# Performance work log

Hardware: AMD Instinct MI355X
Metric: run time of the kernel (lower is better)

Reference implementation:

```python
import jax, jax.numpy as jnp
import numpy as np
import math

B = 32
TS_LEN = 8192
DSEG = 32
S = TS_LEN // DSEG          # 256 segments
DM = 256                    # dim_model
NBITS = 8                   # bits of the bucket signature (synthetic _compute_index)
NBUCKETS = 2 ** NBITS       # 256 ragged-vocab buckets, made uniform here
W = 512                     # words per bucket (uniform -> vocabulary_dist[b] = b*W)
NHAAR = 6                   # min(log2(S)=8, max_haar_depth=6)
LMAX = 13                   # full haar depth of wavedec on length-8192 signal


def _layer_norm(x, eps=1e-5):
    m = x.mean(-1, keepdims=True)
    v = ((x - m) ** 2).mean(-1, keepdims=True)
    return (x - m) / jnp.sqrt(v + eps)


def _pos_emb():
    # sinusoidal positional embedding, matches the torch buffer construction
    pos = jnp.arange(S, dtype=jnp.float32)[:, None]
    div = jnp.exp(jnp.arange(0, DM, 2, dtype=jnp.float32) * (-math.log(10000.0) / DM))
    pe = jnp.zeros((S, DM), jnp.float32)
    pe = pe.at[:, 0::2].set(jnp.sin(pos * div))
    pe = pe.at[:, 1::2].set(jnp.cos(pos * div))
    return pe


def setup_inputs() -> dict:
    key = jax.random.key(0)
    k1, k2, k3, k4 = jax.random.split(key, 4)
    x = jax.random.normal(k1, (B, TS_LEN), jnp.float32)
    # candidate words live in [0,1] (they are compared against min-max-normalized segments)
    vocab_table = jax.random.uniform(k2, (NBUCKETS, W, DSEG), dtype=jnp.float32)
    word_emb = jax.random.normal(k3, (NBUCKETS * W, DM), jnp.float32)
    haar_emb = jax.random.normal(k4, (NHAAR + 1, DM), jnp.float32)
    return {"x": x, "vocab_table": vocab_table, "word_emb": word_emb, "haar_emb": haar_emb}


def reference(x, vocab_table, word_emb, haar_emb):
    # ---- _adjust: input length == ts_len -> identity, att_mask all ones ----
    att_mask = jnp.ones((B, S), jnp.int32)

    # ---- compute_word_embedding (vectorized over batch and segments) ----
    segs = x.reshape(B, S, DSEG)
    smin = segs.min(-1, keepdims=True)
    smax = segs.max(-1, keepdims=True)
    seg_norm = (segs - smin) / (smax - smin + 1e-8)
    # synthetic _compute_index: 8-bit signature (chunk mean above segment mean)
    chunk_means = segs.reshape(B, S, NBITS, DSEG // NBITS).mean(-1)       # [B,S,8]
    bits = (chunk_means > segs.mean(-1, keepdims=True)).astype(jnp.int32)
    bucket = (bits * (2 ** jnp.arange(NBITS, dtype=jnp.int32))).sum(-1)   # [B,S]
    cand = vocab_table[bucket]                                            # [B,S,W,DSEG]
    dist = jnp.abs(cand - seg_norm[:, :, None, :]).sum(-1)                # [B,S,W] L1 cdist
    best = jnp.argmin(dist, axis=-1)                                      # [B,S]
    word_embed = word_emb[bucket * W + best]                              # [B,S,DM]

    # ---- compute_haar_embedding (pywt.wavedec with 'haar', first NHAAR+1 coeffs) ----
    a = x
    details = []
    sqrt2 = jnp.float32(math.sqrt(2.0))
    for _ in range(LMAX):
        even = a[:, 0::2]
        odd = a[:, 1::2]
        details.append((even - odd) / sqrt2)
        a = (even + odd) / sqrt2
    coeffs = [a] + details[::-1]                # [cA_L, cD_L, ..., cD_1]
    taken = coeffs[: NHAAR + 1]
    rows = [jnp.repeat(c, S // c.shape[1], axis=1) for c in taken]        # each [B,S]
    haar_matrix = jnp.stack(rows, axis=-1)                                # [B,S,NHAAR+1]
    haar_matrix = haar_matrix * att_mask[..., None].astype(haar_matrix.dtype)
    haar_embed = haar_matrix @ haar_emb                                   # [B,S,DM]
    haar_embed = _layer_norm(haar_embed)

    out = word_embed + haar_embed + _pos_emb()
    out = _layer_norm(out)
    return (out, att_mask)
```

## Files before the change

### kernel.cpp

```cpp
#include <hip/hip_runtime.h>
#include <math.h>

#define BB 32
#define TS 8192
#define DSEG 32
#define SS 256
#define DM 256
#define W 512
#define CAP 1024

__global__ __launch_bounds__(256) void prep_haar_pe_kernel(
    const float* __restrict__ x,
    float* __restrict__ segn_g,
    unsigned char* __restrict__ bucketc,
    unsigned long long* __restrict__ bestkey,
    float* __restrict__ hout,
    float* __restrict__ pe_g)
{
    const int blk = blockIdx.x;
    const int t = threadIdx.x;

    if (blk < 1024) {
        const int segBase = blk * 8;
        __shared__ float sseg[8][32];
        sseg[t >> 5][t & 31] = x[(size_t)segBase * 32 + t];
        __syncthreads();

        const int hw = t >> 5;
        const int h = hw & 1;
        const int l = t & 31;
        const int seg = segBase + hw;

        float v = sseg[hw][l];
        float mn = v, mx = v, sm = v;
#pragma unroll
        for (int m = 1; m <= 16; m <<= 1) {
            mn = fminf(mn, __shfl_xor(mn, m));
            mx = fmaxf(mx, __shfl_xor(mx, m));
            sm += __shfl_xor(sm, m);
        }
        float mean = sm * (1.0f / 32.0f);
        float cm = 0.0f;
        if (l < 8) {
            cm = ((sseg[hw][4 * l] + sseg[hw][4 * l + 1]) + sseg[hw][4 * l + 2]) +
                 sseg[hw][4 * l + 3];
            cm *= 0.25f;
        }
        unsigned long long bal = __ballot(l < 8 && cm > mean);
        segn_g[(size_t)seg * 32 + l] = (v - mn) / (mx - mn + 1e-8f);
        if (l == 0) bucketc[seg] = (unsigned char)((bal >> (h * 32)) & 0xFF);
        if (l == 1) bestkey[seg] = ~0ULL;
    } else if (blk < 1056) {
        const int b = blk - 1024;
        const int lane = t;
        if (lane >= 64) return;
        const float* xb = x + (size_t)b * TS + (size_t)lane * 128;
        const float is2 = 0.70710678118654752440f;

        float a[64];
#pragma unroll
        for (int i = 0; i < 32; ++i) {
            float4 u = *(const float4*)(xb + 4 * i);
            a[2 * i + 0] = (u.x + u.y) * is2;
            a[2 * i + 1] = (u.z + u.w) * is2;
        }
#pragma unroll
        for (int len = 64; len > 1; len >>= 1) {
#pragma unroll
            for (int j = 0; j < (len >> 1); ++j)
                a[j] = (a[2 * j] + a[2 * j + 1]) * is2;
        }
        float val = a[0];
        float* ob = hout + b * 64;
#pragma unroll
        for (int len = 64; len > 1; len >>= 1) {
            float e = __shfl(val, 2 * lane);
            float o = __shfl(val, 2 * lane + 1);
            int half = len >> 1;
            if (lane < half) {
                ob[half + lane] = (e - o) * is2;
                val = (e + o) * is2;
            }
        }
        if (lane == 0) ob[0] = val;
    } else {
        const int s = blk - 1056;
        const float cexp = -9.210340371976184f / 256.0f;
        float dv = expf((float)(t & ~1) * cexp);
        float ang = (float)s * dv;
        pe_g[s * DM + t] = (t & 1) ? cosf(ang) : sinf(ang);
    }
}

__global__ __launch_bounds__(512) void search_kernel(
    const float* __restrict__ vocab,
    const float* __restrict__ segn_g,
    const unsigned char* __restrict__ bucketc,
    unsigned long long* __restrict__ bestkey)
{
    const int bucket = blockIdx.x >> 1;
    const int half = blockIdx.x & 1;
    const int t = threadIdx.x;
    const int lane = t & 63;
    const int wid = t >> 6;

    __shared__ float vsh[256 * 32];
    __shared__ int list[CAP];
    __shared__ int cnt;
    if (t == 0) cnt = 0;
    __syncthreads();

    {
        uint4 v16 = ((const uint4*)bucketc)[t];
        const unsigned char* pb = (const unsigned char*)&v16;
        int base = t * 16;
#pragma unroll
        for (int j = 0; j < 16; ++j) {
            if (pb[j] == (unsigned char)bucket) {
                int p = atomicAdd(&cnt, 1);
                if (p < CAP) list[p] = base + j;
            }
        }
    }

    const float* vb = vocab + ((size_t)bucket * W + (size_t)half * 256) * DSEG;
#pragma unroll 2
    for (int f = t; f < 2048; f += 512) {
        int r = f >> 3, q = f & 7;
        float4 u = ((const float4*)vb)[f];
        int sq = q ^ (r & 7);
        *(float4*)&vsh[r * 32 + sq * 4] = u;
    }
    __syncthreads();

    int n = cnt; if (n > CAP) n = CAP;
    for (int i = 2 * wid; i < n; i += 16) {
        const int segA = list[i];
        const bool hasB = (i + 1 < n);
        const int segB = hasB ? list[i + 1] : segA;
        const float* spA = segn_g + (size_t)segA * 32;
        const float* spB = segn_g + (size_t)segB * 32;
        float svA[32], svB[32];
#pragma unroll
        for (int d = 0; d < 32; ++d) { svA[d] = spA[d]; svB[d] = spB[d]; }

        unsigned long long bestA = ~0ULL, bestB = ~0ULL;
#pragma unroll
        for (int c = 0; c < 4; ++c) {
            const int r = c * 64 + lane;
            float dA = 0.0f, dB = 0.0f;
#pragma unroll
            for (int q = 0; q < 8; ++q) {
                float4 u = *(const float4*)&vsh[r * 32 + ((q ^ (r & 7)) * 4)];
                dA += fabsf(u.x - svA[4 * q + 0]);
                dA += fabsf(u.y - svA[4 * q + 1]);
                dA += fabsf(u.z - svA[4 * q + 2]);
                dA += fabsf(u.w - svA[4 * q + 3]);
                dB += fabsf(u.x - svB[4 * q + 0]);
                dB += fabsf(u.y - svB[4 * q + 1]);
                dB += fabsf(u.z - svB[4 * q + 2]);
                dB += fabsf(u.w - svB[4 * q + 3]);
            }
            unsigned w = (unsigned)(half * 256 + r);
            unsigned long long kA =
                ((unsigned long long)__float_as_uint(dA) << 32) | w;
            unsigned long long kB =
                ((unsigned long long)__float_as_uint(dB) << 32) | w;
            if (kA < bestA) bestA = kA;
            if (kB < bestB) bestB = kB;
        }
#pragma unroll
        for (int m = 1; m < 64; m <<= 1) {
            unsigned long long oA = __shfl_xor(bestA, m);
            unsigned long long oB = __shfl_xor(bestB, m);
            if (oA < bestA) bestA = oA;
            if (oB < bestB) bestB = oB;
        }
        if (lane == 0) {
            atomicMin(bestkey + segA, bestA);
            if (hasB) atomicMin(bestkey + segB, bestB);
        }
    }
}

__global__ __launch_bounds__(256) void out_kernel(
    const float* __restrict__ wemb,
    const float* __restrict__ hemb,
    const float* __restrict__ hcoef,
    const float* __restrict__ pe_g,
    const unsigned char* __restrict__ bucketc,
    const unsigned long long* __restrict__ bestkey,
    float* __restrict__ out)
{
    const int bs = (blockIdx.x << 2) + (threadIdx.x >> 6);
    const int lane = threadIdx.x & 63;
    const int b = bs >> 8;
    const int s = bs & 255;

    const int bucket = bucketc[bs];
    const int bestw = (int)(unsigned)(bestkey[bs] & 0xFFFFFFFFull);

    const float* hb = hcoef + b * 64;
    float hk[7];
    hk[0] = hb[0];
#pragma unroll
    for (int k = 1; k <= 6; ++k)
        hk[k] = hb[(1 << (k - 1)) + (s >> (8 - (k - 1)))];

    float h0 = 0.f, h1 = 0.f, h2 = 0.f, h3 = 0.f;
#pragma unroll
    for (int k = 0; k < 7; ++k) {
        float4 he = ((const float4*)(hemb + k * DM))[lane];
        h0 += hk[k] * he.x; h1 += hk[k] * he.y;
        h2 += hk[k] * he.z; h3 += hk[k] * he.w;
    }

    float sm = ((h0 + h1) + h2) + h3;
    float sq = ((h0 * h0 + h1 * h1) + h2 * h2) + h3 * h3;
#pragma unroll
    for (int m = 1; m < 64; m <<= 1) {
        sm += __shfl_xor(sm, m);
        sq += __shfl_xor(sq, m);
    }
    float mh = sm * (1.0f / 256.0f);
    float vh = fmaxf(sq * (1.0f / 256.0f) - mh * mh, 0.0f);
    float rs = 1.0f / sqrtf(vh + 1e-5f);
    float n0 = (h0 - mh) * rs, n1 = (h1 - mh) * rs;
    float n2 = (h2 - mh) * rs, n3 = (h3 - mh) * rs;

    const size_t row = (size_t)bucket * W + (size_t)bestw;
    float4 wv = ((const float4*)(wemb + row * DM))[lane];

    float4 pv = ((const float4*)(pe_g + s * DM))[lane];

    float o0 = wv.x + n0 + pv.x;
    float o1 = wv.y + n1 + pv.y;
    float o2 = wv.z + n2 + pv.z;
    float o3 = wv.w + n3 + pv.w;

    float sm2 = ((o0 + o1) + o2) + o3;
    float sq2 = ((o0 * o0 + o1 * o1) + o2 * o2) + o3 * o3;
#pragma unroll
    for (int m = 1; m < 64; m <<= 1) {
        sm2 += __shfl_xor(sm2, m);
        sq2 += __shfl_xor(sq2, m);
    }
    float mo = sm2 * (1.0f / 256.0f);
    float vo = fmaxf(sq2 * (1.0f / 256.0f) - mo * mo, 0.0f);
    float rs2 = 1.0f / sqrtf(vo + 1e-5f);

    float4 res;
    res.x = (o0 - mo) * rs2; res.y = (o1 - mo) * rs2;
    res.z = (o2 - mo) * rs2; res.w = (o3 - mo) * rs2;
    ((float4*)(out + (size_t)bs * DM))[lane] = res;
    if (lane == 0) out[(size_t)BB * SS * DM + bs] = 1.0f;
}

extern "C" void kernel_launch(void* const* d_in, const int* in_sizes, int n_in,
                              void* d_out, int out_size, void* d_ws, size_t ws_size,
                              hipStream_t stream) {
    const float* x     = (const float*)d_in[0];
    const float* vocab = (const float*)d_in[1];
    const float* wemb  = (const float*)d_in[2];
    const float* hemb  = (const float*)d_in[3];
    float* out = (float*)d_out;

    char* ws = (char*)d_ws;
    float* segn                  = (float*)ws;
    unsigned long long* bestkey  = (unsigned long long*)(ws + 1048576);
    unsigned char* bucketc       = (unsigned char*)(ws + 1048576 + 65536);
    float* hco                   = (float*)(ws + 1048576 + 65536 + 8192);
    float* pe_g                  = (float*)(ws + 1048576 + 65536 + 16384);

    prep_haar_pe_kernel<<<1312, 256, 0, stream>>>(x, segn, bucketc, bestkey,
                                                  hco, pe_g);
    search_kernel<<<512, 512, 0, stream>>>(vocab, segn, bucketc, bestkey);
    out_kernel<<<2048, 256, 0, stream>>>(wemb, hemb, hco, pe_g, bucketc,
                                         bestkey, out);
}
```

Before: 206.9 us.

## Build per-bucket segment lists in prep kernel and split search eightfold

The prep kernel now appends each segment to a global per-bucket list through an atomic counter, zeroed by a memset, so the search kernel no longer scans all bucket bytes in every block. The search is split into 8 blocks per bucket, each holding 64 candidate words in shared memory, which gives 2048 smaller blocks with more parallelism and less shared memory per block. The cost is an extra memset launch, more global atomics on bucket counters, and each segment's data being reloaded by 8 blocks instead of 2.

Result: slower. 232.8 us (+12.6%).

```diff
diff --git a/kernel.cpp b/kernel.cpp
--- a/kernel.cpp
+++ b/kernel.cpp
@@ -7,7 +7,9 @@
 #define SS 256
 #define DM 256
 #define W 512
-#define CAP 1024
+#define SPLIT 8
+#define CAND (W / SPLIT)
+#define CAP 2048
 
 __global__ __launch_bounds__(256) void prep_haar_pe_kernel(
     const float* __restrict__ x,
@@ -15,7 +17,9 @@
     unsigned char* __restrict__ bucketc,
     unsigned long long* __restrict__ bestkey,
     float* __restrict__ hout,
-    float* __restrict__ pe_g)
+    float* __restrict__ pe_g,
+    int* __restrict__ bucket_cnt,
+    int* __restrict__ list_g)
 {
     const int blk = blockIdx.x;
     const int t = threadIdx.x;
@@ -48,7 +52,12 @@
         }
         unsigned long long bal = __ballot(l < 8 && cm > mean);
         segn_g[(size_t)seg * 32 + l] = (v - mn) / (mx - mn + 1e-8f);
-        if (l == 0) bucketc[seg] = (unsigned char)((bal >> (h * 32)) & 0xFF);
+        if (l == 0) {
+            int bucket = (int)((bal >> (h * 32)) & 0xFF);
+            bucketc[seg] = (unsigned char)bucket;
+            int slot = atomicAdd(bucket_cnt + bucket, 1);
+            if (slot < CAP) list_g[bucket * CAP + slot] = seg;
+        }
         if (l == 1) bestkey[seg] = ~0ULL;
     } else if (blk < 1056) {
         const int b = blk - 1024;
@@ -95,80 +104,62 @@
 __global__ __launch_bounds__(512) void search_kernel(
     const float* __restrict__ vocab,
     const float* __restrict__ segn_g,
-    const unsigned char* __restrict__ bucketc,
+    const int* __restrict__ bucket_cnt,
+    const int* __restrict__ list_g,
     unsigned long long* __restrict__ bestkey)
 {
-    const int bucket = blockIdx.x >> 1;
-    const int half = blockIdx.x & 1;
+    const int bucket = blockIdx.x >> 3;
+    const int part = blockIdx.x & 7;
     const int t = threadIdx.x;
     const int lane = t & 63;
     const int wid = t >> 6;
 
-    __shared__ float vsh[256 * 32];
-    __shared__ int list[CAP];
-    __shared__ int cnt;
-    if (t == 0) cnt = 0;
-    __syncthreads();
+    __shared__ float vsh[CAND * 32];
 
     {
-        uint4 v16 = ((const uint4*)bucketc)[t];
-        const unsigned char* pb = (const unsigned char*)&v16;
-        int base = t * 16;
-#pragma unroll
-        for (int j = 0; j < 16; ++j) {
-            if (pb[j] == (unsigned char)bucket) {
-                int p = atomicAdd(&cnt, 1);
-                if (p < CAP) list[p] = base + j;
-            }
-        }
-    }
-
-    const float* vb = vocab + ((size_t)bucket * W + (size_t)half * 256) * DSEG;
-#pragma unroll 2
-    for (int f = t; f < 2048; f += 512) {
-        int r = f >> 3, q = f & 7;
-        float4 u = ((const float4*)vb)[f];
+        const float* vb =
+            vocab + ((size_t)bucket * W + (size_t)part * CAND) * DSEG;
+        int r = t >> 3, q = t & 7;
+        float4 u = ((const float4*)vb)[t];
         int sq = q ^ (r & 7);
         *(float4*)&vsh[r * 32 + sq * 4] = u;
     }
+    int n = bucket_cnt[bucket];
+    if (n > CAP) n = CAP;
     __syncthreads();
-
-    int n = cnt; if (n > CAP) n = CAP;
+    if (n == 0) return;
+
+    const int* lst = list_g + bucket * CAP;
+    const unsigned wbase = (unsigned)(part * CAND);
+
     for (int i = 2 * wid; i < n; i += 16) {
-        const int segA = list[i];
+        const int segA = lst[i];
         const bool hasB = (i + 1 < n);
-        const int segB = hasB ? list[i + 1] : segA;
+        const int segB = hasB ? lst[i + 1] : segA;
         const float* spA = segn_g + (size_t)segA * 32;
         const float* spB = segn_g + (size_t)segB * 32;
         float svA[32], svB[32];
 #pragma unroll
         for (int d = 0; d < 32; ++d) { svA[d] = spA[d]; svB[d] = spB[d]; }
 
-        unsigned long long bestA = ~0ULL, bestB = ~0ULL;
-#pragma unroll
-        for (int c = 0; c < 4; ++c) {
-            const int r = c * 64 + lane;
-            float dA = 0.0f, dB = 0.0f;
-#pragma unroll
-            for (int q = 0; q < 8; ++q) {
-                float4 u = *(const float4*)&vsh[r * 32 + ((q ^ (r & 7)) * 4)];
-                dA += fabsf(u.x - svA[4 * q + 0]);
-                dA += fabsf(u.y - svA[4 * q + 1]);
-                dA += fabsf(u.z - svA[4 * q + 2]);
-                dA += fabsf(u.w - svA[4 * q + 3]);
-                dB += fabsf(u.x - svB[4 * q + 0]);
-                dB += fabsf(u.y - svB[4 * q + 1]);
-                dB += fabsf(u.z - svB[4 * q + 2]);
-                dB += fabsf(u.w - svB[4 * q + 3]);
-            }
-            unsigned w = (unsigned)(half * 256 + r);
-            unsigned long long kA =
-                ((unsigned long long)__float_as_uint(dA) << 32) | w;
-            unsigned long long kB =
-                ((unsigned long long)__float_as_uint(dB) << 32) | w;
-            if (kA < bestA) bestA = kA;
-            if (kB < bestB) bestB = kB;
-        }
+        const int r = lane;
+        float dA = 0.0f, dB = 0.0f;
+#pragma unroll
+        for (int q = 0; q < 8; ++q) {
+            float4 u = *(const float4*)&vsh[r * 32 + ((q ^ (r & 7)) * 4)];
+            dA += fabsf(u.x - svA[4 * q + 0]);
+            dA += fabsf(u.y - svA[4 * q + 1]);
+            dA += fabsf(u.z - svA[4 * q + 2]);
+            dA += fabsf(u.w - svA[4 * q + 3]);
+            dB += fabsf(u.x - svB[4 * q + 0]);
+            dB += fabsf(u.y - svB[4 * q + 1]);
+            dB += fabsf(u.z - svB[4 * q + 2]);
+            dB += fabsf(u.w - svB[4 * q + 3]);
+        }
+        unsigned long long bestA =
+            ((unsigned long long)__float_as_uint(dA) << 32) | (wbase + lane);
+        unsigned long long bestB =
+            ((unsigned long long)__float_as_uint(dB) << 32) | (wbase + lane);
 #pragma unroll
         for (int m = 1; m < 64; m <<= 1) {
             unsigned long long oA = __shfl_xor(bestA, m);
@@ -271,10 +262,14 @@
     unsigned char* bucketc       = (unsigned char*)(ws + 1048576 + 65536);
     float* hco                   = (float*)(ws + 1048576 + 65536 + 8192);
     float* pe_g                  = (float*)(ws + 1048576 + 65536 + 16384);
-
+    int* bucket_cnt              = (int*)(ws + 1048576 + 65536 + 16384 + 262144);
+    int* list_g                  = (int*)(ws + 1048576 + 65536 + 16384 + 262144 + 1024);
+
+    hipMemsetAsync(bucket_cnt, 0, 256 * sizeof(int), stream);
     prep_haar_pe_kernel<<<1312, 256, 0, stream>>>(x, segn, bucketc, bestkey,
-                                                  hco, pe_g);
-    search_kernel<<<512, 512, 0, stream>>>(vocab, segn, bucketc, bestkey);
+                                                  hco, pe_g, bucket_cnt, list_g);
+    search_kernel<<<256 * SPLIT, 512, 0, stream>>>(vocab, segn, bucket_cnt,
+                                                   list_g, bestkey);
     out_kernel<<<2048, 256, 0, stream>>>(wemb, hemb, hco, pe_g, bucketc,
                                          bestkey, out);
 }
```
